# Kernel optimization log

Measured on AMD Instinct MI355X. Metric: run time of the kernel, lower is better.

Reference implementation:

```python
import jax, jax.numpy as jnp
from jax import lax
import numpy as np

B, S, H = 8, 512, 768


def setup_inputs() -> dict:
    key = jax.random.key(0)
    ks = jax.random.split(key, 8)
    outputs = jax.random.normal(ks[0], (B, S, H), dtype=jnp.float32)
    starts = jax.random.randint(ks[1], (B,), S // 4, 3 * S // 4)
    mask = jnp.stack([starts, jnp.full((B,), S, dtype=starts.dtype)], axis=1)  # [B,2]
    sc = 1.0 / np.sqrt(H)
    Wa_w = jax.random.normal(ks[2], (H, H), dtype=jnp.float32) * sc
    Wa_b = jax.random.normal(ks[3], (H,), dtype=jnp.float32) * sc
    Ua_w = jax.random.normal(ks[4], (H, H), dtype=jnp.float32) * sc
    Ua_b = jax.random.normal(ks[5], (H,), dtype=jnp.float32) * sc
    Va_w = jax.random.normal(ks[6], (1, H), dtype=jnp.float32) * sc
    Va_b = jax.random.normal(ks[7], (1,), dtype=jnp.float32) * sc
    return {"outputs": outputs, "mask": mask, "Wa_w": Wa_w, "Wa_b": Wa_b,
            "Ua_w": Ua_w, "Ua_b": Ua_b, "Va_w": Va_w, "Va_b": Va_b}


def reference(outputs, mask, Wa_w, Wa_b, Ua_w, Ua_b, Va_w, Va_b):
    # outputs: [B,S,H]; mask[:,0] = start (source = tokens [0:start], summary = [start:S])
    b, s, h = outputs.shape
    Wq = jnp.einsum('bsh,oh->bso', outputs, Wa_w) + Wa_b  # query proj, [B,S,H]
    Uk = jnp.einsum('bsh,oh->bso', outputs, Ua_w) + Ua_b  # key proj,   [B,S,H]
    va = Va_w[0]  # [H]
    vb = Va_b[0]

    # Stream over query token positions to avoid a [B,S,S,H] tanh intermediate.
    def step(_, wq_t):  # wq_t: [B,H]
        m = jnp.tanh(wq_t[:, None, :] + Uk)          # [B,S,H]
        sc_t = jnp.einsum('bkh,h->bk', m, va) + vb   # [B,S]
        return None, sc_t

    _, scores = lax.scan(step, None, jnp.swapaxes(Wq, 0, 1))  # [S(query token), B, S(key)]
    scores = jnp.swapaxes(scores, 0, 1)  # [B, S_token, S_key]

    start = mask[:, 0]                              # [B]
    j = jnp.arange(s)
    # summary query j corresponds to token index start + j
    t_idx = jnp.clip(start[:, None] + j[None, :], 0, s - 1)            # [B,S]
    sc = jnp.take_along_axis(scores, t_idx[:, :, None], axis=1)       # [B,S,S]
    key_mask = (j[None, :] < start[:, None])                           # [B,S] valid source keys
    q_mask = (j[None, :] < (s - start)[:, None])                       # [B,S] valid summary queries

    sc = jnp.where(key_mask[:, None, :], sc, -1e30)
    w = jax.nn.softmax(sc, axis=-1)
    # zero out exactly where the torch code leaves zeros
    attentions = w * key_mask[:, None, :].astype(w.dtype) * q_mask[:, :, None].astype(w.dtype)
    contexts = jnp.einsum('bjk,bkh->bjh', attentions, outputs)
    return attentions, contexts
```

## Files before the change

### kernel.cpp

```cpp
#include <hip/hip_runtime.h>

typedef float  f32x4   __attribute__((ext_vector_type(4)));
typedef short  short8  __attribute__((ext_vector_type(8)));
typedef unsigned short ushort8 __attribute__((ext_vector_type(8)));

constexpr int kB = 8;
constexpr int kS = 512;
constexpr int kH = 768;
constexpr int kJM = 384;

constexpr float kTanhScale = 2.8853900817779268f;

__device__ __forceinline__ float native_exp2(float x) {
    float r; asm("v_exp_f32 %0, %1" : "=v"(r) : "v"(x)); return r;
}

__device__ __forceinline__ unsigned short bf16_rtn(float x) {
    unsigned u = __float_as_uint(x);
    unsigned r = u + 0x7FFFu + ((u >> 16) & 1u);
    return (unsigned short)(r >> 16);
}

__device__ __forceinline__ float waveMax(float v) {
#pragma unroll
    for (int off = 32; off > 0; off >>= 1) v = fmaxf(v, __shfl_xor(v, off, 64));
    return v;
}
__device__ __forceinline__ float waveSum(float v) {
#pragma unroll
    for (int off = 32; off > 0; off >>= 1) v += __shfl_xor(v, off, 64);
    return v;
}

__global__ __launch_bounds__(256) void k0_convert(
    const float* __restrict__ X, const float* __restrict__ Wa, const float* __restrict__ Ua,
    unsigned short* __restrict__ Xhi, unsigned short* __restrict__ Xlo,
    unsigned short* __restrict__ Wahi, unsigned short* __restrict__ Uahi)
{
    const int i4 = blockIdx.x * 256 + threadIdx.x;
    if (i4 < 786432) {
        float4 v = *(const float4*)(X + (size_t)i4 * 4);
        unsigned short h[4], l[4];
#pragma unroll
        for (int c = 0; c < 4; ++c) {
            float x = (&v.x)[c];
            h[c] = bf16_rtn(x);
            float hf = __uint_as_float((unsigned)h[c] << 16);
            l[c] = bf16_rtn(x - hf);
        }
        *(ushort4*)(Xhi + (size_t)i4 * 4) = make_ushort4(h[0], h[1], h[2], h[3]);
        *(ushort4*)(Xlo + (size_t)i4 * 4) = make_ushort4(l[0], l[1], l[2], l[3]);
    } else {
        const float* src; unsigned short* hi; int off;
        if (i4 < 933888) { src = Wa; hi = Wahi; off = i4 - 786432; }
        else             { src = Ua; hi = Uahi; off = i4 - 933888; }
        float4 v = *(const float4*)(src + (size_t)off * 4);
        *(ushort4*)(hi + (size_t)off * 4) =
            make_ushort4(bf16_rtn(v.x), bf16_rtn(v.y), bf16_rtn(v.z), bf16_rtn(v.w));
    }
}

__global__ __launch_bounds__(256) void k1_mfma(
    const unsigned short* __restrict__ Xhi, const unsigned short* __restrict__ Xlo,
    const unsigned short* __restrict__ W0hi, const unsigned short* __restrict__ W1hi,
    const float* __restrict__ b0, const float* __restrict__ b1,
    const int* __restrict__ mask,
    float* __restrict__ Eqc, float* __restrict__ EkTc)
{
    __shared__ char smem[49664];
    unsigned short* Ahi = (unsigned short*)smem;
    unsigned short* Alo = (unsigned short*)(smem + 10240);
    unsigned short* Bhi = (unsigned short*)(smem + 20480);

    const int z = blockIdx.z;
    const unsigned short* Whi = z ? W1hi : W0hi;
    const float* bias = z ? b1 : b0;

    const int m0 = blockIdx.y * 128;
    const int n0 = blockIdx.x * 96;
    const int t  = threadIdx.x;
    const int bI = m0 >> 9;
    const int lb = m0 & (kS - 1);
    const int start = mask[2 * bI];

    if (z == 0) { if (lb + 128 <= start) return; }
    else        { if (lb >= start) return; }

    const int ar = t >> 1, ko = (t & 1) << 4;
    const bool doB = (ar < 96);
    const size_t aoff = (size_t)(m0 + ar) * kH + ko;
    const size_t woff = (size_t)(n0 + ar) * kH + ko;

    const int wid = t >> 6, lane = t & 63;
    const int wr = wid >> 1, wc = wid & 1;
    const int lr = lane & 15, lk = (lane >> 4) << 3;

    f32x4 acc[4][3];
#pragma unroll
    for (int mi = 0; mi < 4; ++mi)
#pragma unroll
        for (int ni = 0; ni < 3; ++ni)
#pragma unroll
            for (int r = 0; r < 4; ++r) acc[mi][ni][r] = 0.0f;

    for (int h0 = 0; h0 < kH; h0 += 32) {
        ushort8 ah0 = *(const ushort8*)(Xhi + aoff + h0);
        ushort8 ah1 = *(const ushort8*)(Xhi + aoff + h0 + 8);
        ushort8 al0 = *(const ushort8*)(Xlo + aoff + h0);
        ushort8 al1 = *(const ushort8*)(Xlo + aoff + h0 + 8);
        ushort8 bh0, bh1;
        if (doB) {
            bh0 = *(const ushort8*)(Whi + woff + h0);
            bh1 = *(const ushort8*)(Whi + woff + h0 + 8);
        }
        __syncthreads();
        *(ushort8*)(Ahi + ar * 40 + ko)     = ah0;
        *(ushort8*)(Ahi + ar * 40 + ko + 8) = ah1;
        *(ushort8*)(Alo + ar * 40 + ko)     = al0;
        *(ushort8*)(Alo + ar * 40 + ko + 8) = al1;
        if (doB) {
            *(ushort8*)(Bhi + ar * 40 + ko)     = bh0;
            *(ushort8*)(Bhi + ar * 40 + ko + 8) = bh1;
        }
        __syncthreads();

        short8 ah[4], al_[4], bh[3];
#pragma unroll
        for (int mi = 0; mi < 4; ++mi) {
            const int row = wr * 64 + mi * 16 + lr;
            ah[mi]  = *(const short8*)(Ahi + row * 40 + lk);
            al_[mi] = *(const short8*)(Alo + row * 40 + lk);
        }
#pragma unroll
        for (int ni = 0; ni < 3; ++ni) {
            const int row = wc * 48 + ni * 16 + lr;
            bh[ni] = *(const short8*)(Bhi + row * 40 + lk);
        }
#pragma unroll
        for (int mi = 0; mi < 4; ++mi)
#pragma unroll
            for (int ni = 0; ni < 3; ++ni)
                acc[mi][ni] = __builtin_amdgcn_mfma_f32_16x16x32_bf16(ah[mi], bh[ni], acc[mi][ni], 0, 0, 0);
#pragma unroll
        for (int mi = 0; mi < 4; ++mi)
#pragma unroll
            for (int ni = 0; ni < 3; ++ni)
                acc[mi][ni] = __builtin_amdgcn_mfma_f32_16x16x32_bf16(al_[mi], bh[ni], acc[mi][ni], 0, 0, 0);
    }

    if (z == 0) {
#pragma unroll
        for (int mi = 0; mi < 4; ++mi)
#pragma unroll
            for (int ni = 0; ni < 3; ++ni) {
                const int ml = lb + wr * 64 + mi * 16 + ((lane >> 4) << 2);
                const int ng = n0 + wc * 48 + ni * 16 + lr;
                const float bn = bias[ng];
#pragma unroll
                for (int r = 0; r < 4; ++r) {
                    const int jj = ml + r - start;
                    if (jj >= 0)
                        Eqc[((size_t)bI * kJM + jj) * kH + ng] =
                            native_exp2((acc[mi][ni][r] + bn) * kTanhScale);
                }
            }
    } else {
        __syncthreads();
        float* stg = (float*)smem;
#pragma unroll
        for (int mi = 0; mi < 4; ++mi)
#pragma unroll
            for (int ni = 0; ni < 3; ++ni) {
                const int ml = wr * 64 + mi * 16 + ((lane >> 4) << 2);
                const int nl = wc * 48 + ni * 16 + lr;
                const float bn = bias[n0 + nl];
#pragma unroll
                for (int r = 0; r < 4; ++r)
                    stg[(ml + r) * 97 + nl] = native_exp2((acc[mi][ni][r] + bn) * kTanhScale);
            }
        __syncthreads();
        const int s4 = (t & 31) << 2, hb_ = t >> 5;
        const int sg = lb + s4;
#pragma unroll
        for (int u = 0; u < 12; ++u) {
            const int h = (u << 3) + hb_;
            float o[4] = { stg[(s4 + 0) * 97 + h], stg[(s4 + 1) * 97 + h],
                           stg[(s4 + 2) * 97 + h], stg[(s4 + 3) * 97 + h] };
            float* dst = EkTc + ((size_t)bI * kH + n0 + h) * kJM + sg;
            if (sg + 3 < start) {
                *(float4*)dst = make_float4(o[0], o[1], o[2], o[3]);
            } else {
#pragma unroll
                for (int e2 = 0; e2 < 4; ++e2)
                    if (sg + e2 < start) dst[e2] = o[e2];
            }
        }
    }
}

__global__ void k2a_worklist(const int* __restrict__ mask, int* __restrict__ wl)
{
    __shared__ int ne[kB], off[kB];
    const int tid = threadIdx.x;
    if (tid < kB) {
        int start = mask[2 * tid];
        ne[tid] = ((kS - start + 3) >> 2) * ((start + 63) >> 6) * 2;
    }
    __syncthreads();
    if (tid == 0) {
        int s = 0;
        for (int b = 0; b < kB; ++b) { off[b] = s; s += ne[b]; }
        wl[0] = s;
    }
    __syncthreads();
    for (int b = 0; b < kB; ++b) {
        int start = mask[2 * b];
        int nkw = (start + 63) >> 6;
        int nkc = nkw * 2;
        int n = ne[b], base = off[b];
        for (int t = tid; t < n; t += blockDim.x) {
            int jt = t / nkc;
            int r = t - jt * nkc;
            int kt = r >> 1, c = r & 1;
            wl[1 + base + t] = (b << 16) | (jt << 8) | (kt << 1) | c;
        }
    }
}

__global__ __launch_bounds__(256) void k2_scores(
    const float* __restrict__ Eqc, const float* __restrict__ EkTc,
    const float* __restrict__ va, const int* __restrict__ mask,
    const int* __restrict__ wl, float* __restrict__ part0, float* __restrict__ part1)
{
    constexpr int JT = 4;
    const int ntiles = wl[0];
    const int lane = threadIdx.x & 63;
    const int wslot = (blockIdx.x << 2) | (threadIdx.x >> 6);
    const int nslots = gridDim.x << 2;

    for (int w = wslot; w < ntiles; w += nslots) {
        const int e = __builtin_amdgcn_readfirstlane(wl[1 + w]);
        const int b = e >> 16, jt = (e >> 8) & 255, ktc = e & 255;
        const int kt = ktc >> 1, c = ktc & 1;
        const int start = __builtin_amdgcn_readfirstlane(mask[2 * b]);
        const int jmax = kS - start;
        const int j0 = jt * JT, k0 = kt << 6;
        const int hbase = c * 384;

        const float* eqr[JT];
#pragma unroll
        for (int j = 0; j < JT; ++j)
            eqr[j] = Eqc + ((size_t)b * kJM + j0 + j) * kH + hbase;
        const float* ekp = EkTc + ((size_t)b * kH + hbase) * kJM + k0 + lane;
        const float* vap = va + hbase;

        float acc[JT] = {};
        float eA[8], eB[8];
#pragma unroll
        for (int c2 = 0; c2 < 8; ++c2) eA[c2] = ekp[(size_t)c2 * kJM];
#pragma unroll
        for (int c2 = 0; c2 < 8; ++c2) eB[c2] = ekp[(size_t)(8 + c2) * kJM];

        for (int h0 = 0; h0 < 384; h0 += 16) {
            const bool more = (h0 + 16) < 384;
            float nA[8], nB[8];
            if (more) {
#pragma unroll
                for (int c2 = 0; c2 < 8; ++c2) nA[c2] = ekp[(size_t)(h0 + 16 + c2) * kJM];
            }
#pragma unroll
            for (int c2 = 0; c2 < 8; ++c2) {
                const float vc = vap[h0 + c2];
#pragma unroll
                for (int j = 0; j < JT; ++j) {
                    float r = __builtin_amdgcn_rcpf(fmaf(eqr[j][h0 + c2], eA[c2], 1.0f));
                    acc[j] = fmaf(vc, r, acc[j]);
                }
            }
            if (more) {
#pragma unroll
                for (int c2 = 0; c2 < 8; ++c2) nB[c2] = ekp[(size_t)(h0 + 24 + c2) * kJM];
            }
#pragma unroll
            for (int c2 = 0; c2 < 8; ++c2) {
                const float vc = vap[h0 + 8 + c2];
#pragma unroll
                for (int j = 0; j < JT; ++j) {
                    float r = __builtin_amdgcn_rcpf(fmaf(eqr[j][h0 + 8 + c2], eB[c2], 1.0f));
                    acc[j] = fmaf(vc, r, acc[j]);
                }
            }
            if (more) {
#pragma unroll
                for (int c2 = 0; c2 < 8; ++c2) { eA[c2] = nA[c2]; eB[c2] = nB[c2]; }
            }
        }

        float* srow = (c ? part1 : part0) + ((size_t)b * kS + j0) * kS + k0 + lane;
#pragma unroll
        for (int j = 0; j < JT; ++j)
            if (j0 + j < jmax) srow[(size_t)j * kS] = -2.0f * acc[j];
    }
}

__global__ __launch_bounds__(256) void k3_softmax(
    float* __restrict__ attn, const float* __restrict__ part1,
    const int* __restrict__ mask)
{
    const int bx = blockIdx.x;
    const int b = bx >> 9;
    const int j = bx & (kS - 1);
    const int start = mask[2 * b];
    float* row = attn + ((size_t)b * kS + j) * kS;
    const int tid = threadIdx.x;

    if (j >= kS - start) {
        row[tid] = 0.0f;
        row[tid + 256] = 0.0f;
        return;
    }

    const float* p1row = part1 + ((size_t)b * kS + j) * kS;
    float v0 = (tid < start) ? row[tid] + p1row[tid] : -1e30f;
    float v1 = (tid + 256 < start) ? row[tid + 256] + p1row[tid + 256] : -1e30f;

    __shared__ float red[4];
    const int wid = tid >> 6;

    float m = waveMax(fmaxf(v0, v1));
    if ((tid & 63) == 0) red[wid] = m;
    __syncthreads();
    m = fmaxf(fmaxf(red[0], red[1]), fmaxf(red[2], red[3]));
    __syncthreads();

    float e0 = (tid < start) ? __expf(v0 - m) : 0.0f;
    float e1 = (tid + 256 < start) ? __expf(v1 - m) : 0.0f;
    float s = waveSum(e0 + e1);
    if ((tid & 63) == 0) red[wid] = s;
    __syncthreads();
    s = red[0] + red[1] + red[2] + red[3];

    float inv = __builtin_amdgcn_rcpf(s);
    row[tid] = e0 * inv;
    row[tid + 256] = e1 * inv;
}

__global__ __launch_bounds__(256) void k4_context(
    const float* __restrict__ attn, const float* __restrict__ outs,
    const int* __restrict__ mask, float* __restrict__ ctx)
{
    const int b = blockIdx.z;
    const int start = mask[2 * b];
    const int kmax = (start + 15) & ~15;
    const int m0 = blockIdx.y * 64;
    const int n0 = blockIdx.x * 64;

    __shared__ float As[16][68];
    __shared__ float Bs[16][68];

    const int tid = threadIdx.x;
    const int lrow = tid >> 2;
    const int lk4  = (tid & 3) << 2;
    const int brow = tid >> 4;
    const int bh4  = (tid & 15) << 2;
    const int is = tid >> 4;
    const int js = tid & 15;

    const float* arow = attn + ((size_t)b * kS + m0 + lrow) * kS + lk4;
    const float* bbase = outs + (size_t)b * kS * kH + n0 + bh4;

    float acc[4][4] = {};

    for (int k0 = 0; k0 < kmax; k0 += 16) {
        float4 av = *(const float4*)(arow + k0);
        float4 bv = *(const float4*)(bbase + (size_t)(k0 + brow) * kH);
        __syncthreads();
        As[lk4 + 0][lrow] = av.x;
        As[lk4 + 1][lrow] = av.y;
        As[lk4 + 2][lrow] = av.z;
        As[lk4 + 3][lrow] = av.w;
        *(float4*)&Bs[brow][bh4] = bv;
        __syncthreads();
#pragma unroll
        for (int kk = 0; kk < 16; ++kk) {
            const float* ap = &As[kk][is << 2];
            const float* bp = &Bs[kk][js << 2];
            float aa[4], bb[4];
#pragma unroll
            for (int c = 0; c < 4; ++c) { aa[c] = ap[c]; bb[c] = bp[c]; }
#pragma unroll
            for (int i = 0; i < 4; ++i)
#pragma unroll
                for (int j = 0; j < 4; ++j)
                    acc[i][j] = fmaf(aa[i], bb[j], acc[i][j]);
        }
    }

#pragma unroll
    for (int i = 0; i < 4; ++i) {
        int row = m0 + (is << 2) + i;
        float4 o = {acc[i][0], acc[i][1], acc[i][2], acc[i][3]};
        *(float4*)(ctx + ((size_t)b * kS + row) * kH + n0 + (js << 2)) = o;
    }
}

extern "C" void kernel_launch(void* const* d_in, const int* in_sizes, int n_in,
                              void* d_out, int out_size, void* d_ws, size_t ws_size,
                              hipStream_t stream)
{
    const float* outputs = (const float*)d_in[0];
    const int*   mask    = (const int*)d_in[1];
    const float* Wa_w    = (const float*)d_in[2];
    const float* Wa_b    = (const float*)d_in[3];
    const float* Ua_w    = (const float*)d_in[4];
    const float* Ua_b    = (const float*)d_in[5];
    const float* Va_w    = (const float*)d_in[6];

    float* attn = (float*)d_out;
    float* ctx  = attn + (size_t)kB * kS * kS;

    unsigned short* Xhi  = (unsigned short*)ctx;
    unsigned short* Xlo  = Xhi + (size_t)kB * kS * kH;
    unsigned short* Wahi = (unsigned short*)attn;
    unsigned short* Uahi = Wahi + (size_t)kH * kH;
    float* part1 = ctx;

    int* wl = (int*)d_ws;
    float* Eqc  = (float*)((char*)d_ws + 131072);
    float* EkTc = Eqc + (size_t)kB * kJM * kH;

    k0_convert<<<dim3(4224), 256, 0, stream>>>(
        outputs, Wa_w, Ua_w, Xhi, Xlo, Wahi, Uahi);

    k1_mfma<<<dim3(kH / 96, (kB * kS) / 128, 2), 256, 0, stream>>>(
        Xhi, Xlo, Wahi, Uahi, Wa_b, Ua_b, mask, Eqc, EkTc);

    k2a_worklist<<<dim3(1), 256, 0, stream>>>(mask, wl);
    k2_scores<<<dim3(1024), 256, 0, stream>>>(Eqc, EkTc, Va_w, mask, wl, attn, part1);

    k3_softmax<<<dim3(kB * kS), 256, 0, stream>>>(attn, part1, mask);

    k4_context<<<dim3(kH / 64, kS / 64, kB), 256, 0, stream>>>(attn, outputs, mask, ctx);
}
```

Baseline: 145.2 us.

## Move context GEMM to split-bf16 MFMA with transposed bf16 operands

Replaces the fp32 FMA tiled context GEMM with a matrix-core kernel that uses hi/lo bf16 splitting (three MFMAs per tile) to keep near-fp32 accuracy. Softmax now also writes bf16 hi/lo copies of the attention rows. A new kernel transposes and splits `outputs` into bf16 hi/lo in reused workspace. The launch grid of the scores kernel is also doubled. The intent is to cut the FMA-bound cost of the context product. In exchange it adds extra conversion passes and memory traffic, and gives slightly lower precision than pure fp32.

```diff
diff --git a/kernel.cpp b/kernel.cpp
--- a/kernel.cpp
+++ b/kernel.cpp
@@ -303,9 +303,48 @@
     }
 }
 
+__global__ __launch_bounds__(256) void k4a_convert(
+    const float* __restrict__ X,
+    unsigned short* __restrict__ OThi, unsigned short* __restrict__ OTlo)
+{
+    __shared__ float st[64][65];
+    const int b = blockIdx.z;
+    const int s0 = blockIdx.y * 64;
+    const int h0 = blockIdx.x * 64;
+    const int t = threadIdx.x;
+
+    const int sr = t >> 2, hc = (t & 3) << 4;
+    const float* src = X + ((size_t)b * kS + s0 + sr) * kH + h0 + hc;
+#pragma unroll
+    for (int q = 0; q < 4; ++q) {
+        float4 v = *(const float4*)(src + 4 * q);
+        st[sr][hc + 4 * q + 0] = v.x;
+        st[sr][hc + 4 * q + 1] = v.y;
+        st[sr][hc + 4 * q + 2] = v.z;
+        st[sr][hc + 4 * q + 3] = v.w;
+    }
+    __syncthreads();
+
+    const int hr = t >> 2, sc = (t & 3) << 4;
+    unsigned short h[16], l[16];
+#pragma unroll
+    for (int i = 0; i < 16; ++i) {
+        float x = st[sc + i][hr];
+        h[i] = bf16_rtn(x);
+        float hf = __uint_as_float((unsigned)h[i] << 16);
+        l[i] = bf16_rtn(x - hf);
+    }
+    const size_t dst = ((size_t)b * kH + h0 + hr) * kJM + s0 + sc;
+    *(ushort8*)(OThi + dst)     = *(ushort8*)(h);
+    *(ushort8*)(OThi + dst + 8) = *(ushort8*)(h + 8);
+    *(ushort8*)(OTlo + dst)     = *(ushort8*)(l);
+    *(ushort8*)(OTlo + dst + 8) = *(ushort8*)(l + 8);
+}
+
 __global__ __launch_bounds__(256) void k3_softmax(
     float* __restrict__ attn, const float* __restrict__ part1,
-    const int* __restrict__ mask)
+    const int* __restrict__ mask,
+    unsigned short* __restrict__ Ahi, unsigned short* __restrict__ Alo)
 {
     const int bx = blockIdx.x;
     const int b = bx >> 9;
@@ -313,10 +352,13 @@
     const int start = mask[2 * b];
     float* row = attn + ((size_t)b * kS + j) * kS;
     const int tid = threadIdx.x;
+    const size_t abase = ((size_t)b * kS + j) * kJM;
 
     if (j >= kS - start) {
         row[tid] = 0.0f;
         row[tid + 256] = 0.0f;
+        Ahi[abase + tid] = 0; Alo[abase + tid] = 0;
+        if (tid < 128) { Ahi[abase + 256 + tid] = 0; Alo[abase + 256 + tid] = 0; }
         return;
     }
 
@@ -341,67 +383,121 @@
     s = red[0] + red[1] + red[2] + red[3];
 
     float inv = __builtin_amdgcn_rcpf(s);
-    row[tid] = e0 * inv;
-    row[tid + 256] = e1 * inv;
-}
-
-__global__ __launch_bounds__(256) void k4_context(
-    const float* __restrict__ attn, const float* __restrict__ outs,
+    float a0 = e0 * inv, a1 = e1 * inv;
+    row[tid] = a0;
+    row[tid + 256] = a1;
+
+    unsigned short h0 = bf16_rtn(a0);
+    Ahi[abase + tid] = h0;
+    Alo[abase + tid] = bf16_rtn(a0 - __uint_as_float((unsigned)h0 << 16));
+    if (tid < 128) {
+        unsigned short h1 = bf16_rtn(a1);
+        Ahi[abase + 256 + tid] = h1;
+        Alo[abase + 256 + tid] = bf16_rtn(a1 - __uint_as_float((unsigned)h1 << 16));
+    }
+}
+
+__global__ __launch_bounds__(256) void k4_mfma(
+    const unsigned short* __restrict__ Ahi_g, const unsigned short* __restrict__ Alo_g,
+    const unsigned short* __restrict__ Bhi_g, const unsigned short* __restrict__ Blo_g,
     const int* __restrict__ mask, float* __restrict__ ctx)
 {
-    const int b = blockIdx.z;
-    const int start = mask[2 * b];
-    const int kmax = (start + 15) & ~15;
-    const int m0 = blockIdx.y * 64;
-    const int n0 = blockIdx.x * 64;
-
-    __shared__ float As[16][68];
-    __shared__ float Bs[16][68];
-
-    const int tid = threadIdx.x;
-    const int lrow = tid >> 2;
-    const int lk4  = (tid & 3) << 2;
-    const int brow = tid >> 4;
-    const int bh4  = (tid & 15) << 2;
-    const int is = tid >> 4;
-    const int js = tid & 15;
-
-    const float* arow = attn + ((size_t)b * kS + m0 + lrow) * kS + lk4;
-    const float* bbase = outs + (size_t)b * kS * kH + n0 + bh4;
-
-    float acc[4][4] = {};
-
-    for (int k0 = 0; k0 < kmax; k0 += 16) {
-        float4 av = *(const float4*)(arow + k0);
-        float4 bv = *(const float4*)(bbase + (size_t)(k0 + brow) * kH);
+    __shared__ char smem[35840];
+    unsigned short* Ahi = (unsigned short*)smem;
+    unsigned short* Alo = (unsigned short*)(smem + 10240);
+    unsigned short* Bhi = (unsigned short*)(smem + 20480);
+    unsigned short* Blo = (unsigned short*)(smem + 28160);
+
+    const int m0 = blockIdx.y * 128;
+    const int n0 = blockIdx.x * 96;
+    const int t  = threadIdx.x;
+    const int bI = m0 >> 9;
+    const int jb = m0 & (kS - 1);
+    const int start = mask[2 * bI];
+    const int kmax = (start + 31) & ~31;
+
+    const int ar = t >> 1, ko = (t & 1) << 4;
+    const bool doB = (ar < 96);
+    const size_t aoff = ((size_t)bI * kS + jb + ar) * kJM + ko;
+    const size_t woff = ((size_t)bI * kH + n0 + ar) * kJM + ko;
+
+    const int wid = t >> 6, lane = t & 63;
+    const int wr = wid >> 1, wc = wid & 1;
+    const int lr = lane & 15, lk = (lane >> 4) << 3;
+
+    f32x4 acc[4][3];
+#pragma unroll
+    for (int mi = 0; mi < 4; ++mi)
+#pragma unroll
+        for (int ni = 0; ni < 3; ++ni)
+#pragma unroll
+            for (int r = 0; r < 4; ++r) acc[mi][ni][r] = 0.0f;
+
+    for (int k0 = 0; k0 < kmax; k0 += 32) {
+        ushort8 ah0 = *(const ushort8*)(Ahi_g + aoff + k0);
+        ushort8 ah1 = *(const ushort8*)(Ahi_g + aoff + k0 + 8);
+        ushort8 al0 = *(const ushort8*)(Alo_g + aoff + k0);
+        ushort8 al1 = *(const ushort8*)(Alo_g + aoff + k0 + 8);
+        ushort8 bh0, bh1, bl0, bl1;
+        if (doB) {
+            bh0 = *(const ushort8*)(Bhi_g + woff + k0);
+            bh1 = *(const ushort8*)(Bhi_g + woff + k0 + 8);
+            bl0 = *(const ushort8*)(Blo_g + woff + k0);
+            bl1 = *(const ushort8*)(Blo_g + woff + k0 + 8);
+        }
         __syncthreads();
-        As[lk4 + 0][lrow] = av.x;
-        As[lk4 + 1][lrow] = av.y;
-        As[lk4 + 2][lrow] = av.z;
-        As[lk4 + 3][lrow] = av.w;
-        *(float4*)&Bs[brow][bh4] = bv;
+        *(ushort8*)(Ahi + ar * 40 + ko)     = ah0;
+        *(ushort8*)(Ahi + ar * 40 + ko + 8) = ah1;
+        *(ushort8*)(Alo + ar * 40 + ko)     = al0;
+        *(ushort8*)(Alo + ar * 40 + ko + 8) = al1;
+        if (doB) {
+            *(ushort8*)(Bhi + ar * 40 + ko)     = bh0;
+            *(ushort8*)(Bhi + ar * 40 + ko + 8) = bh1;
+            *(ushort8*)(Blo + ar * 40 + ko)     = bl0;
+            *(ushort8*)(Blo + ar * 40 + ko + 8) = bl1;
+        }
         __syncthreads();
-#pragma unroll
-        for (int kk = 0; kk < 16; ++kk) {
-            const float* ap = &As[kk][is << 2];
-            const float* bp = &Bs[kk][js << 2];
-            float aa[4], bb[4];
-#pragma unroll
-            for (int c = 0; c < 4; ++c) { aa[c] = ap[c]; bb[c] = bp[c]; }
-#pragma unroll
-            for (int i = 0; i < 4; ++i)
-#pragma unroll
-                for (int j = 0; j < 4; ++j)
-                    acc[i][j] = fmaf(aa[i], bb[j], acc[i][j]);
-        }
-    }
-
-#pragma unroll
-    for (int i = 0; i < 4; ++i) {
-        int row = m0 + (is << 2) + i;
-        float4 o = {acc[i][0], acc[i][1], acc[i][2], acc[i][3]};
-        *(float4*)(ctx + ((size_t)b * kS + row) * kH + n0 + (js << 2)) = o;
-    }
+
+        short8 ah[4], al_[4], bh[3], bl[3];
+#pragma unroll
+        for (int mi = 0; mi < 4; ++mi) {
+            const int row = wr * 64 + mi * 16 + lr;
+            ah[mi]  = *(const short8*)(Ahi + row * 40 + lk);
+            al_[mi] = *(const short8*)(Alo + row * 40 + lk);
+        }
+#pragma unroll
+        for (int ni = 0; ni < 3; ++ni) {
+            const int row = wc * 48 + ni * 16 + lr;
+            bh[ni] = *(const short8*)(Bhi + row * 40 + lk);
+            bl[ni] = *(const short8*)(Blo + row * 40 + lk);
+        }
+#pragma unroll
+        for (int mi = 0; mi < 4; ++mi)
+#pragma unroll
+            for (int ni = 0; ni < 3; ++ni)
+                acc[mi][ni] = __builtin_amdgcn_mfma_f32_16x16x32_bf16(ah[mi], bh[ni], acc[mi][ni], 0, 0, 0);
+#pragma unroll
+        for (int mi = 0; mi < 4; ++mi)
+#pragma unroll
+            for (int ni = 0; ni < 3; ++ni)
+                acc[mi][ni] = __builtin_amdgcn_mfma_f32_16x16x32_bf16(al_[mi], bh[ni], acc[mi][ni], 0, 0, 0);
+#pragma unroll
+        for (int mi = 0; mi < 4; ++mi)
+#pragma unroll
+            for (int ni = 0; ni < 3; ++ni)
+                acc[mi][ni] = __builtin_amdgcn_mfma_f32_16x16x32_bf16(ah[mi], bl[ni], acc[mi][ni], 0, 0, 0);
+    }
+
+#pragma unroll
+    for (int mi = 0; mi < 4; ++mi)
+#pragma unroll
+        for (int ni = 0; ni < 3; ++ni) {
+            const int mg = m0 + wr * 64 + mi * 16 + ((lane >> 4) << 2);
+            const int ng = n0 + wc * 48 + ni * 16 + lr;
+#pragma unroll
+            for (int r = 0; r < 4; ++r)
+                ctx[(size_t)(mg + r) * kH + ng] = acc[mi][ni][r];
+        }
 }
 
 extern "C" void kernel_launch(void* const* d_in, const int* in_sizes, int n_in,
@@ -429,6 +525,11 @@
     float* Eqc  = (float*)((char*)d_ws + 131072);
     float* EkTc = Eqc + (size_t)kB * kJM * kH;
 
+    unsigned short* AttnHi = (unsigned short*)Eqc;
+    unsigned short* AttnLo = AttnHi + (size_t)kB * kS * kJM;
+    unsigned short* OThi   = (unsigned short*)EkTc;
+    unsigned short* OTlo   = OThi + (size_t)kB * kH * kJM;
+
     k0_convert<<<dim3(4224), 256, 0, stream>>>(
         outputs, Wa_w, Ua_w, Xhi, Xlo, Wahi, Uahi);
 
@@ -436,9 +537,12 @@
         Xhi, Xlo, Wahi, Uahi, Wa_b, Ua_b, mask, Eqc, EkTc);
 
     k2a_worklist<<<dim3(1), 256, 0, stream>>>(mask, wl);
-    k2_scores<<<dim3(1024), 256, 0, stream>>>(Eqc, EkTc, Va_w, mask, wl, attn, part1);
-
-    k3_softmax<<<dim3(kB * kS), 256, 0, stream>>>(attn, part1, mask);
-
-    k4_context<<<dim3(kH / 64, kS / 64, kB), 256, 0, stream>>>(attn, outputs, mask, ctx);
-}
+    k2_scores<<<dim3(2048), 256, 0, stream>>>(Eqc, EkTc, Va_w, mask, wl, attn, part1);
+
+    k4a_convert<<<dim3(kH / 64, kJM / 64, kB), 256, 0, stream>>>(outputs, OThi, OTlo);
+
+    k3_softmax<<<dim3(kB * kS), 256, 0, stream>>>(attn, part1, mask, AttnHi, AttnLo);
+
+    k4_mfma<<<dim3(kH / 96, (kB * kS) / 128), 256, 0, stream>>>(
+        AttnHi, AttnLo, OThi, OTlo, mask, ctx);
+}
```

Result: no change. 146.6 us (+1.0%).
